# Kernel optimization log

Measured on AMD Instinct MI355X. Metric: run time of the kernel, lower is better.

## Reference

```python
import jax, jax.numpy as jnp
import numpy as np

P, M, DG, F, H, DH = 2000, 150, 2000, 256, 4, 64
N1, N2 = P + M, P + DG          # adj1 nodes (patient+med), adj2 nodes (patient+diag)
E1, E2, EGP, EGM = 137600, 256000, 64000, 4800
GNN_LAYERS = 2
SA_HID = 128


def setup_inputs() -> dict:
    key = jax.random.key(0)
    ks = jax.random.split(key, 32)
    ri = lambda k, n, hi: jax.random.randint(k, (n,), 0, hi, dtype=jnp.int32)
    rn = lambda k, shape, scale: (jax.random.normal(k, shape, dtype=jnp.float32) * scale)
    inp = {
        'adj1_rows': ri(ks[0], E1, N1), 'adj1_cols': ri(ks[1], E1, N1),
        'adj1_vals': jax.random.uniform(ks[2], (E1,), dtype=jnp.float32),
        'adj2_rows': ri(ks[3], E2, N2), 'adj2_cols': ri(ks[4], E2, N2),
        'adj2_vals': jax.random.uniform(ks[5], (E2,), dtype=jnp.float32),
        'g0_src': ri(ks[6], EGP, P), 'g0_dst': ri(ks[7], EGP, P),
        'g1_src': ri(ks[8], EGP, P), 'g1_dst': ri(ks[9], EGP, P),
        'g2_src': ri(ks[10], EGM, M), 'g2_dst': ri(ks[11], EGM, M),
        'g3_src': ri(ks[12], EGM, M), 'g3_dst': ri(ks[13], EGM, M),
        'keepRate': 1,
        # learned parameters (xavier-ish scales)
        'pEmbed': rn(ks[14], (P, F), 0.05),
        'mEmbed': rn(ks[15], (M, F), 0.05),
        'dEmbed': rn(ks[16], (DG, F), 0.05),
        'gat_W': rn(ks[17], (4, F, H * DH), (2.0 / (F + H * DH)) ** 0.5),
        'gat_al': rn(ks[18], (4, H, DH), 0.1),
        'gat_ar': rn(ks[19], (4, H, DH), 0.1),
        'gat_b': jnp.zeros((4, H * DH), dtype=jnp.float32),
        'sa_W1': rn(ks[20], (H * DH, SA_HID), (2.0 / (H * DH + SA_HID)) ** 0.5),
        'sa_b1': jnp.zeros((SA_HID,), dtype=jnp.float32),
        'sa_W2': rn(ks[21], (SA_HID, 1), 0.1),
        'out_W': rn(ks[22], (2 * F, M), (2.0 / (2 * F + M)) ** 0.5),
        'out_b': jnp.zeros((M,), dtype=jnp.float32),
    }
    return inp


def _spmm(rows, cols, vals, x, n):
    # sparse adj @ x via gather + segment_sum
    return jax.ops.segment_sum(vals[:, None] * x[cols], rows, num_segments=n)


def _seg_softmax(e, seg, n):
    m = jax.ops.segment_max(e, seg, num_segments=n)          # [n, H]
    ex = jnp.exp(e - m[seg])
    s = jax.ops.segment_sum(ex, seg, num_segments=n)
    return ex / (s[seg] + 1e-9)


def _gat(h, W, al, ar, b, src, dst, n):
    # DGL GATConv, feat/attn dropout = 0, negative_slope = 0.2, activation = elu
    feat = (h @ W).reshape(n, H, DH)                          # [n, H, DH]
    el = (feat * al[None]).sum(-1)                            # [n, H]
    er = (feat * ar[None]).sum(-1)
    e = jax.nn.leaky_relu(el[src] + er[dst], negative_slope=0.2)  # [E, H]
    alpha = _seg_softmax(e, dst, n)                           # softmax over in-edges per dst
    out = jax.ops.segment_sum(alpha[:, :, None] * feat[src], dst, num_segments=n)
    out = out + b.reshape(1, H, DH)
    return jax.nn.elu(out).reshape(n, H * DH)


def _sem_att(z, W1, b1, W2):
    # z: [N, K, F]; shared projection; beta over K meta-paths
    w = (jnp.tanh(z @ W1 + b1) @ W2).mean(0)                  # [K, 1]
    beta = jax.nn.softmax(w, axis=0)                          # [K, 1]
    return (beta[None] * z).sum(1)                            # [N, F]


def reference(adj1_rows, adj1_cols, adj1_vals, adj2_rows, adj2_cols, adj2_vals,
              g0_src, g0_dst, g1_src, g1_dst, g2_src, g2_dst, g3_src, g3_dst,
              keepRate, pEmbed, mEmbed, dEmbed, gat_W, gat_al, gat_ar, gat_b,
              sa_W1, sa_b1, sa_W2, out_W, out_b):
    embeds1 = jnp.concatenate([pEmbed, mEmbed], axis=0)       # [N1, F]
    embeds2 = jnp.concatenate([pEmbed, dEmbed], axis=0)       # [N2, F]
    lat1, lat2 = embeds1, embeds2
    acc1 = jnp.zeros_like(embeds1)
    acc2 = jnp.zeros_like(embeds2)
    for _ in range(GNN_LAYERS):
        lat1 = jax.nn.leaky_relu(_spmm(adj1_rows, adj1_cols, adj1_vals, lat1, N1), negative_slope=0.5)
        lat2 = jax.nn.leaky_relu(_spmm(adj2_rows, adj2_cols, adj2_vals, lat2, N2), negative_slope=0.5)
        acc1 = acc1 + lat1
        acc2 = acc2 + lat2
    p1, m_gcn = acc1[:P], acc1[P:]
    p2, d_gcn = acc2[:P], acc2[P:]

    e0 = _gat(p1, gat_W[0], gat_al[0], gat_ar[0], gat_b[0], g0_src, g0_dst, P)
    e1 = _gat(p2, gat_W[1], gat_al[1], gat_ar[1], gat_b[1], g1_src, g1_dst, P)
    e2 = _gat(m_gcn, gat_W[2], gat_al[2], gat_ar[2], gat_b[2], g2_src, g2_dst, M)
    e3 = _gat(m_gcn, gat_W[3], gat_al[3], gat_ar[3], gat_b[3], g3_src, g3_dst, M)

    patient = _sem_att(jnp.stack([e0, e1], axis=1), sa_W1, sa_b1, sa_W2)  # [P, F]
    med = _sem_att(jnp.stack([e2, e3], axis=1), sa_W1, sa_b1, sa_W2)      # [M, F]

    # broadcasted pairwise concat -> ReLU -> Linear -> sum over pairing axis
    pm = jnp.concatenate([
        jnp.broadcast_to(patient[:, None, :], (P, M, F)),
        jnp.broadcast_to(med[None, :, :], (P, M, F)),
    ], axis=-1).reshape(P * M, 2 * F)
    simi = (jax.nn.relu(pm) @ out_W + out_b).reshape(P, M, M)
    simi_pm = simi.sum(axis=1)                                # [P, M]
    return (simi_pm, d_gcn, med, m_gcn, patient)
```

## Files before the change

kernel.cpp:

```cpp
#include <hip/hip_runtime.h>
#include <cmath>
#include <cstdint>

constexpr int P  = 2000, M = 150, DG = 2000, F = 256, H = 4, DH = 64;
constexpr int N1 = P + M;
constexpr int N2 = P + DG;
constexpr int E1 = 137600, E2 = 256000, EGP = 64000, EGM = 4800;
constexpr int SA_HID = 128;

constexpr int HO1 = E1, HO2 = E1 + E2, HO3 = HO2 + EGP, HO4 = HO3 + EGP,
              HO5 = HO4 + EGM, HOE = HO5 + EGM;

__global__ void k_hist_all(const int* __restrict__ a1r, const int* __restrict__ a2r,
                           const int* __restrict__ d0, const int* __restrict__ d1,
                           const int* __restrict__ d2, const int* __restrict__ d3,
                           int* __restrict__ c1, int* __restrict__ c2,
                           int* __restrict__ cg0, int* __restrict__ cg1,
                           int* __restrict__ cg2, int* __restrict__ cg3) {
  int i = blockIdx.x * 256 + threadIdx.x;
  if (i >= HOE) return;
  if (i < HO1)      atomicAdd(&c1[a1r[i]], 1);
  else if (i < HO2) atomicAdd(&c2[a2r[i - HO1]], 1);
  else if (i < HO3) atomicAdd(&cg0[d0[i - HO2]], 1);
  else if (i < HO4) atomicAdd(&cg1[d1[i - HO3]], 1);
  else if (i < HO5) atomicAdd(&cg2[d2[i - HO4]], 1);
  else              atomicAdd(&cg3[d3[i - HO5]], 1);
}

struct ScanArgs { const int* cnt[6]; int* off[6]; int* cur[6]; int n[6]; };

__global__ void k_scan_all(ScanArgs a) {
  int b = blockIdx.x;
  const int* cnt = a.cnt[b]; int* off = a.off[b]; int* cur = a.cur[b]; int n = a.n[b];
  __shared__ int part[256];
  int t = threadIdx.x;
  int chunk = (n + 255) >> 8;
  int base = t * chunk;
  int s = 0;
  for (int i = 0; i < chunk; ++i) { int id = base + i; if (id < n) s += cnt[id]; }
  part[t] = s;
  __syncthreads();
  for (int d = 1; d < 256; d <<= 1) {
    int v = (t >= d) ? part[t - d] : 0;
    __syncthreads();
    part[t] += v;
    __syncthreads();
  }
  int run = (t == 0) ? 0 : part[t - 1];
  for (int i = 0; i < chunk; ++i) {
    int id = base + i;
    if (id < n) { off[id] = run; cur[id] = run; run += cnt[id]; }
  }
  if (t == 0) off[n] = part[255];
}

__global__ void k_scat_all(const int* __restrict__ a1r, const int* __restrict__ a1c,
                           const float* __restrict__ a1v,
                           const int* __restrict__ a2r, const int* __restrict__ a2c,
                           const float* __restrict__ a2v,
                           const int* __restrict__ d0, const int* __restrict__ s0,
                           const int* __restrict__ d1, const int* __restrict__ s1,
                           const int* __restrict__ d2, const int* __restrict__ s2,
                           const int* __restrict__ d3, const int* __restrict__ s3,
                           int* cur1, int* pc1, float* pv1,
                           int* cur2, int* pc2, float* pv2,
                           int* cu0, int* ps0, int* cu1, int* ps1,
                           int* cu2, int* ps2, int* cu3, int* ps3) {
  int i = blockIdx.x * 256 + threadIdx.x;
  if (i >= HOE) return;
  if (i < HO1) {
    int p = atomicAdd(&cur1[a1r[i]], 1); pc1[p] = a1c[i]; pv1[p] = a1v[i];
  } else if (i < HO2) {
    int j = i - HO1;
    int p = atomicAdd(&cur2[a2r[j]], 1); pc2[p] = a2c[j]; pv2[p] = a2v[j];
  } else if (i < HO3) {
    int j = i - HO2; int p = atomicAdd(&cu0[d0[j]], 1); ps0[p] = s0[j];
  } else if (i < HO4) {
    int j = i - HO3; int p = atomicAdd(&cu1[d1[j]], 1); ps1[p] = s1[j];
  } else if (i < HO5) {
    int j = i - HO4; int p = atomicAdd(&cu2[d2[j]], 1); ps2[p] = s2[j];
  } else {
    int j = i - HO5; int p = atomicAdd(&cu3[d3[j]], 1); ps3[p] = s3[j];
  }
}

template<int LAYER>
__global__ __launch_bounds__(256) void k_spmm(
    const int* __restrict__ off1, const int* __restrict__ pc1, const float* __restrict__ pv1,
    const int* __restrict__ off2, const int* __restrict__ pc2, const float* __restrict__ pv2,
    const float* __restrict__ pE, const float* __restrict__ mE, const float* __restrict__ dE,
    float* __restrict__ lat1, float* __restrict__ lat2,
    float* __restrict__ acc1, float* __restrict__ acc2,
    float* __restrict__ out_mgcn, float* __restrict__ out_dgcn) {
  int gw = (blockIdx.x * 256 + threadIdx.x) >> 6;
  if (gw >= N1 + N2) return;
  int lane = threadIdx.x & 63;
  bool g2 = gw >= N1;
  int row = g2 ? gw - N1 : gw;
  const int*   off = g2 ? off2 : off1;
  const int*   pc  = g2 ? pc2  : pc1;
  const float* pv  = g2 ? pv2  : pv1;
  const float* latin = g2 ? lat2 : lat1;
  const float* tailE = g2 ? dE : mE;
  int beg = off[row], end = off[row + 1];
  int fo = lane << 2;
  float4 s = {0.f, 0.f, 0.f, 0.f};
  auto fetch = [&](int c) -> float4 {
    const float* b;
    if (LAYER == 1) b = (c < P) ? (pE + (size_t)c * F) : (tailE + (size_t)(c - P) * F);
    else            b = latin + (size_t)c * F;
    return *(const float4*)(b + fo);
  };
  int i = beg;
  for (; i + 4 <= end; i += 4) {
    int c0 = pc[i], c1 = pc[i + 1], c2 = pc[i + 2], c3 = pc[i + 3];
    float v0 = pv[i], v1 = pv[i + 1], v2 = pv[i + 2], v3 = pv[i + 3];
    float4 a0 = fetch(c0), a1 = fetch(c1), a2 = fetch(c2), a3 = fetch(c3);
    s.x += v0 * a0.x + v1 * a1.x + v2 * a2.x + v3 * a3.x;
    s.y += v0 * a0.y + v1 * a1.y + v2 * a2.y + v3 * a3.y;
    s.z += v0 * a0.z + v1 * a1.z + v2 * a2.z + v3 * a3.z;
    s.w += v0 * a0.w + v1 * a1.w + v2 * a2.w + v3 * a3.w;
  }
  for (; i < end; ++i) {
    int c = pc[i]; float v = pv[i];
    float4 a = fetch(c);
    s.x += v * a.x; s.y += v * a.y; s.z += v * a.z; s.w += v * a.w;
  }
  float4 l;
  l.x = s.x > 0.f ? s.x : 0.5f * s.x;
  l.y = s.y > 0.f ? s.y : 0.5f * s.y;
  l.z = s.z > 0.f ? s.z : 0.5f * s.z;
  l.w = s.w > 0.f ? s.w : 0.5f * s.w;
  if (LAYER == 1) {
    *(float4*)((g2 ? lat2 : lat1) + (size_t)row * F + fo) = l;
  } else {
    float4 b = *(const float4*)(latin + (size_t)row * F + fo);
    float4 a = {b.x + l.x, b.y + l.y, b.z + l.z, b.w + l.w};
    *(float4*)((g2 ? acc2 : acc1) + (size_t)row * F + fo) = a;
    if (row >= P)
      *(float4*)((g2 ? out_dgcn : out_mgcn) + (size_t)(row - P) * F + fo) = a;
  }
}

constexpr int FR  = 4;
constexpr int NB0 = (P + FR - 1) / FR;
constexpr int NB2 = (M + FR - 1) / FR;
constexpr int FEAT_BLOCKS = 2 * NB0 + 2 * NB2;

__global__ __launch_bounds__(256) void k_gat_feat_all(
    const float* __restrict__ acc1, const float* __restrict__ acc2,
    const float* __restrict__ gat_W, const float* __restrict__ gat_al,
    const float* __restrict__ gat_ar,
    float* __restrict__ f0, float* __restrict__ f1,
    float* __restrict__ f2, float* __restrict__ f3,
    float* __restrict__ el, float* __restrict__ er) {
  int b = blockIdx.x;
  int g, rb, n; const float* h; float* fout;
  if (b < NB0)            { g = 0; rb = b;              n = P; h = acc1; fout = f0; }
  else if (b < 2 * NB0)   { g = 1; rb = b - NB0;        n = P; h = acc2; fout = f1; }
  else if (b < 2*NB0+NB2) { g = 2; rb = b - 2 * NB0;    n = M; h = acc1 + (size_t)P * F; fout = f2; }
  else                    { g = 3; rb = b - 2*NB0 - NB2; n = M; h = acc1 + (size_t)P * F; fout = f3; }
  int elo = (g == 0) ? 0 : (g == 1) ? P * H : (g == 2) ? 2 * P * H : (2 * P + M) * H;
  const float* W = gat_W + (size_t)g * F * F;
  __shared__ float hs[FR][F];
  int t = threadIdx.x;
  int r0 = rb * FR;
  {
    int r = t >> 6, ln = t & 63;
    int row = r0 + r;
    float4 v = {0.f, 0.f, 0.f, 0.f};
    if (row < n) v = *(const float4*)(h + (size_t)row * F + (ln << 2));
    *(float4*)&hs[r][ln << 2] = v;
  }
  __syncthreads();
  float acc[FR] = {0.f, 0.f, 0.f, 0.f};
  for (int k = 0; k < F; k += 4) {
    float w0 = W[(size_t)k * F + t],       w1 = W[(size_t)(k + 1) * F + t],
          w2 = W[(size_t)(k + 2) * F + t], w3 = W[(size_t)(k + 3) * F + t];
#pragma unroll
    for (int r = 0; r < FR; ++r) {
      float4 h4 = *(const float4*)&hs[r][k];
      acc[r] += h4.x * w0 + h4.y * w1 + h4.z * w2 + h4.w * w3;
    }
  }
  int head = t >> 6, d = t & 63;
  float av = gat_al[g * H * DH + head * DH + d];
  float rv = gat_ar[g * H * DH + head * DH + d];
#pragma unroll
  for (int r = 0; r < FR; ++r) {
    int row = r0 + r;
    if (row < n) {
      fout[(size_t)row * F + t] = acc[r];
      float cl = acc[r] * av, cr = acc[r] * rv;
      for (int o = 32; o > 0; o >>= 1) {
        cl += __shfl_down(cl, o, 64);
        cr += __shfl_down(cr, o, 64);
      }
      if (d == 0) { el[elo + row * H + head] = cl; er[elo + row * H + head] = cr; }
    }
  }
}

__global__ __launch_bounds__(256) void k_gat_agg_all(
    const int* __restrict__ og0, const int* __restrict__ ps0,
    const int* __restrict__ og1, const int* __restrict__ ps1,
    const int* __restrict__ og2, const int* __restrict__ ps2,
    const int* __restrict__ og3, const int* __restrict__ ps3,
    const float* __restrict__ el, const float* __restrict__ er,
    const float* __restrict__ f0, const float* __restrict__ f1,
    const float* __restrict__ f2, const float* __restrict__ f3,
    const float* __restrict__ gat_b,
    float* __restrict__ e0, float* __restrict__ e1,
    float* __restrict__ e2, float* __restrict__ e3) {
  int gw = (blockIdx.x * 256 + threadIdx.x) >> 6;
  if (gw >= 2 * P + 2 * M) return;
  int lane = threadIdx.x & 63;
  int g, row; const int* off; const int* ps; const float* feat; float* out; int elo;
  if (gw < P)            { g = 0; row = gw;             off = og0; ps = ps0; feat = f0; out = e0; elo = 0; }
  else if (gw < 2 * P)   { g = 1; row = gw - P;         off = og1; ps = ps1; feat = f1; out = e1; elo = P * H; }
  else if (gw < 2*P + M) { g = 2; row = gw - 2 * P;     off = og2; ps = ps2; feat = f2; out = e2; elo = 2 * P * H; }
  else                   { g = 3; row = gw - 2 * P - M; off = og3; ps = ps3; feat = f3; out = e3; elo = (2 * P + M) * H; }
  int head = lane >> 4;
  int fo = lane << 2;
  const float* elb = el + elo;
  float erv = er[elo + row * H + head];
  int beg = off[row], end = off[row + 1];
  float mx = -3.4e38f;
  int i = beg;
  for (; i + 4 <= end; i += 4) {
    int s0 = ps[i], s1 = ps[i + 1], s2 = ps[i + 2], s3 = ps[i + 3];
    float a = elb[s0 * H + head] + erv, b = elb[s1 * H + head] + erv,
          c = elb[s2 * H + head] + erv, d = elb[s3 * H + head] + erv;
    a = a > 0.f ? a : 0.2f * a; b = b > 0.f ? b : 0.2f * b;
    c = c > 0.f ? c : 0.2f * c; d = d > 0.f ? d : 0.2f * d;
    mx = fmaxf(mx, fmaxf(fmaxf(a, b), fmaxf(c, d)));
  }
  for (; i < end; ++i) {
    float a = elb[ps[i] * H + head] + erv;
    a = a > 0.f ? a : 0.2f * a;
    mx = fmaxf(mx, a);
  }
  float ssum = 0.f;
  float4 acc = {0.f, 0.f, 0.f, 0.f};
  i = beg;
  for (; i + 2 <= end; i += 2) {
    int s0 = ps[i], s1 = ps[i + 1];
    float a = elb[s0 * H + head] + erv; a = a > 0.f ? a : 0.2f * a;
    float b = elb[s1 * H + head] + erv; b = b > 0.f ? b : 0.2f * b;
    float x0 = expf(a - mx), x1 = expf(b - mx);
    float4 q0 = *(const float4*)(feat + (size_t)s0 * F + fo);
    float4 q1 = *(const float4*)(feat + (size_t)s1 * F + fo);
    ssum += x0 + x1;
    acc.x += x0 * q0.x + x1 * q1.x;
    acc.y += x0 * q0.y + x1 * q1.y;
    acc.z += x0 * q0.z + x1 * q1.z;
    acc.w += x0 * q0.w + x1 * q1.w;
  }
  for (; i < end; ++i) {
    int s0 = ps[i];
    float a = elb[s0 * H + head] + erv; a = a > 0.f ? a : 0.2f * a;
    float x0 = expf(a - mx);
    float4 q0 = *(const float4*)(feat + (size_t)s0 * F + fo);
    ssum += x0;
    acc.x += x0 * q0.x; acc.y += x0 * q0.y; acc.z += x0 * q0.z; acc.w += x0 * q0.w;
  }
  float inv = 1.f / (ssum + 1e-9f);
  const float* bb = gat_b + g * F + fo;
  float4 v = {acc.x * inv + bb[0], acc.y * inv + bb[1],
              acc.z * inv + bb[2], acc.w * inv + bb[3]};
  v.x = v.x > 0.f ? v.x : expm1f(v.x);
  v.y = v.y > 0.f ? v.y : expm1f(v.y);
  v.z = v.z > 0.f ? v.z : expm1f(v.z);
  v.w = v.w > 0.f ? v.w : expm1f(v.w);
  *(float4*)(out + (size_t)row * F + fo) = v;
}

constexpr int SR  = 8;
constexpr int SB0 = (P + SR - 1) / SR;
constexpr int SB2 = (M + SR - 1) / SR;
constexpr int SEM_BLOCKS = 2 * SB0 + 2 * SB2;

__global__ __launch_bounds__(128) void k_sem_w_all(
    const float* __restrict__ e0, const float* __restrict__ e1,
    const float* __restrict__ e2, const float* __restrict__ e3,
    const float* __restrict__ W1, const float* __restrict__ b1,
    const float* __restrict__ W2, float* __restrict__ w) {
  int b = blockIdx.x;
  int zid, rb, n; const float* z;
  if (b < SB0)            { zid = 0; rb = b;             n = P; z = e0; }
  else if (b < 2 * SB0)   { zid = 1; rb = b - SB0;       n = P; z = e1; }
  else if (b < 2*SB0+SB2) { zid = 2; rb = b - 2 * SB0;   n = M; z = e2; }
  else                    { zid = 3; rb = b - 2*SB0-SB2; n = M; z = e3; }
  __shared__ float zs[SR][F];
  int t = threadIdx.x;
  int r0 = rb * SR;
  for (int q = t; q < SR * 64; q += 128) {
    int r = q >> 6, ln = q & 63;
    int row = r0 + r;
    float4 v = {0.f, 0.f, 0.f, 0.f};
    if (row < n) v = *(const float4*)(z + (size_t)row * F + (ln << 2));
    *(float4*)&zs[r][ln << 2] = v;
  }
  __syncthreads();
  float hid[SR];
#pragma unroll
  for (int r = 0; r < SR; ++r) hid[r] = b1[t];
  for (int k = 0; k < F; k += 4) {
    float w0 = W1[(size_t)k * SA_HID + t],       w1 = W1[(size_t)(k + 1) * SA_HID + t],
          w2 = W1[(size_t)(k + 2) * SA_HID + t], w3 = W1[(size_t)(k + 3) * SA_HID + t];
#pragma unroll
    for (int r = 0; r < SR; ++r) {
      float4 z4 = *(const float4*)&zs[r][k];
      hid[r] += z4.x * w0 + z4.y * w1 + z4.z * w2 + z4.w * w3;
    }
  }
  float w2v = W2[t];
  float local = 0.f;
  for (int r = 0; r < SR; ++r) {
    int row = r0 + r;
    if (row < n) local += tanhf(hid[r]) * w2v;
  }
  for (int o = 32; o > 0; o >>= 1) local += __shfl_down(local, o, 64);
  __shared__ float pp[2];
  if ((t & 63) == 0) pp[t >> 6] = local;
  __syncthreads();
  if (t == 0) atomicAdd(&w[zid], pp[0] + pp[1]);
}

__global__ void k_sem_comb_all(const float* __restrict__ e0, const float* __restrict__ e1,
                               const float* __restrict__ e2, const float* __restrict__ e3,
                               const float* __restrict__ w,
                               float* __restrict__ out_pat, float* __restrict__ out_med) {
  constexpr int Q0 = P * F / 4;
  constexpr int QE = Q0 + M * F / 4;
  int i = blockIdx.x * 256 + threadIdx.x;
  if (i >= QE) return;
  const float4 *z0, *z1; float* out; float inv_n; const float* wp; int j;
  if (i < Q0) { z0 = (const float4*)e0; z1 = (const float4*)e1; out = out_pat; inv_n = 1.f / P; wp = w;     j = i; }
  else        { z0 = (const float4*)e2; z1 = (const float4*)e3; out = out_med; inv_n = 1.f / M; wp = w + 2; j = i - Q0; }
  float m0 = wp[0] * inv_n, m1 = wp[1] * inv_n;
  float mxv = fmaxf(m0, m1);
  float a0 = expf(m0 - mxv), a1 = expf(m1 - mxv);
  float s = 1.f / (a0 + a1);
  a0 *= s; a1 *= s;
  float4 u0 = z0[j], u1 = z1[j];
  float4 r = {a0 * u0.x + a1 * u1.x, a0 * u0.y + a1 * u1.y,
              a0 * u0.z + a1 * u1.z, a0 * u0.w + a1 * u1.w};
  ((float4*)out)[j] = r;
}

__global__ void k_cvec(const float* __restrict__ med, const float* __restrict__ outW,
                       const float* __restrict__ outb, float* __restrict__ c) {
  __shared__ float sv[F];
  int t = threadIdx.x;
  float a = 0.f;
  for (int m = 0; m < M; ++m) { float v = med[(size_t)m * F + t]; a += v > 0.f ? v : 0.f; }
  sv[t] = a;
  __syncthreads();
  if (t < M) {
    float cc = (float)M * outb[t];
    for (int f = 0; f < F; ++f) cc += sv[f] * outW[(size_t)(F + f) * M + t];
    c[t] = cc;
  }
}

constexpr int FIN_R = 8;
__global__ __launch_bounds__(256) void k_final(const float* __restrict__ pat,
                                               const float* __restrict__ outW,
                                               const float* __restrict__ c,
                                               float* __restrict__ simi) {
  __shared__ float psh[FIN_R][F];
  int t = threadIdx.x;
  int r0 = blockIdx.x * FIN_R;
  for (int q = t; q < FIN_R * 64; q += 256) {
    int r = q >> 6, ln = q & 63;
    float4 v = *(const float4*)(pat + (size_t)(r0 + r) * F + (ln << 2));
    v.x = v.x > 0.f ? v.x : 0.f; v.y = v.y > 0.f ? v.y : 0.f;
    v.z = v.z > 0.f ? v.z : 0.f; v.w = v.w > 0.f ? v.w : 0.f;
    *(float4*)&psh[r][ln << 2] = v;
  }
  __syncthreads();
  if (t < M) {
    float acc[FIN_R];
#pragma unroll
    for (int r = 0; r < FIN_R; ++r) acc[r] = 0.f;
    for (int f = 0; f < F; f += 4) {
      float w0 = outW[(size_t)f * M + t],       w1 = outW[(size_t)(f + 1) * M + t],
            w2 = outW[(size_t)(f + 2) * M + t], w3 = outW[(size_t)(f + 3) * M + t];
#pragma unroll
      for (int r = 0; r < FIN_R; ++r) {
        float4 p4 = *(const float4*)&psh[r][f];
        acc[r] += p4.x * w0 + p4.y * w1 + p4.z * w2 + p4.w * w3;
      }
    }
    float cv = c[t];
    for (int r = 0; r < FIN_R; ++r)
      simi[(size_t)(r0 + r) * M + t] = (float)M * acc[r] + cv;
  }
}

extern "C" void kernel_launch(void* const* d_in, const int* in_sizes, int n_in,
                              void* d_out, int out_size, void* d_ws, size_t ws_size,
                              hipStream_t stream) {
  const int*   adj1_rows = (const int*)d_in[0];
  const int*   adj1_cols = (const int*)d_in[1];
  const float* adj1_vals = (const float*)d_in[2];
  const int*   adj2_rows = (const int*)d_in[3];
  const int*   adj2_cols = (const int*)d_in[4];
  const float* adj2_vals = (const float*)d_in[5];
  const int*   g0_src = (const int*)d_in[6];
  const int*   g0_dst = (const int*)d_in[7];
  const int*   g1_src = (const int*)d_in[8];
  const int*   g1_dst = (const int*)d_in[9];
  const int*   g2_src = (const int*)d_in[10];
  const int*   g2_dst = (const int*)d_in[11];
  const int*   g3_src = (const int*)d_in[12];
  const int*   g3_dst = (const int*)d_in[13];
  const float* pE     = (const float*)d_in[15];
  const float* mE     = (const float*)d_in[16];
  const float* dE     = (const float*)d_in[17];
  const float* gat_W  = (const float*)d_in[18];
  const float* gat_al = (const float*)d_in[19];
  const float* gat_ar = (const float*)d_in[20];
  const float* gat_b  = (const float*)d_in[21];
  const float* sa_W1  = (const float*)d_in[22];
  const float* sa_b1  = (const float*)d_in[23];
  const float* sa_W2  = (const float*)d_in[24];
  const float* out_W  = (const float*)d_in[25];
  const float* out_b  = (const float*)d_in[26];

  int* ip = (int*)d_ws;
  int* cnt1 = ip; ip += N1;
  int* cnt2 = ip; ip += N2;
  int* cg0  = ip; ip += P;
  int* cg1  = ip; ip += P;
  int* cg2  = ip; ip += M;
  int* cg3  = ip; ip += M;
  float* wbuf = (float*)ip; ip += 4;
  size_t memset_bytes = (size_t)((char*)ip - (char*)d_ws);
  int* off1 = ip; ip += N1 + 1;  int* cur1 = ip; ip += N1;
  int* pc1  = ip; ip += E1;      float* pv1 = (float*)ip; ip += E1;
  int* off2 = ip; ip += N2 + 1;  int* cur2 = ip; ip += N2;
  int* pc2  = ip; ip += E2;      float* pv2 = (float*)ip; ip += E2;
  int* og0 = ip; ip += P + 1;  int* cu0 = ip; ip += P;  int* ps0 = ip; ip += EGP;
  int* og1 = ip; ip += P + 1;  int* cu1 = ip; ip += P;  int* ps1 = ip; ip += EGP;
  int* og2 = ip; ip += M + 1;  int* cu2 = ip; ip += M;  int* ps2 = ip; ip += EGM;
  int* og3 = ip; ip += M + 1;  int* cu3 = ip; ip += M;  int* ps3 = ip; ip += EGM;
  uintptr_t up = ((uintptr_t)ip + 15) & ~(uintptr_t)15;
  float* fp = (float*)up;
  float* lat1 = fp; fp += (size_t)N1 * F;
  float* lat2 = fp; fp += (size_t)N2 * F;
  float* acc1 = fp; fp += (size_t)N1 * F;
  float* acc2 = fp; fp += (size_t)N2 * F;
  float* f0   = fp; fp += (size_t)P * F;
  float* f1   = fp; fp += (size_t)P * F;
  float* f2   = fp; fp += (size_t)M * F;
  float* f3   = fp; fp += (size_t)M * F;
  float* el   = fp; fp += (size_t)(2 * P + 2 * M) * H;
  float* er   = fp; fp += (size_t)(2 * P + 2 * M) * H;
  float* e0b  = fp; fp += (size_t)P * F;
  float* e1b  = fp; fp += (size_t)P * F;
  float* e2b  = fp; fp += (size_t)M * F;
  float* e3b  = fp; fp += (size_t)M * F;
  float* cbuf = fp; fp += 256;

  float* out_simi = (float*)d_out;
  float* out_dgcn = out_simi + (size_t)P * M;
  float* out_med  = out_dgcn + (size_t)DG * F;
  float* out_mgcn = out_med  + (size_t)M * F;
  float* out_pat  = out_mgcn + (size_t)M * F;

  hipMemsetAsync(d_ws, 0, memset_bytes, stream);

  int eb = (HOE + 255) / 256;
  k_hist_all<<<eb, 256, 0, stream>>>(adj1_rows, adj2_rows, g0_dst, g1_dst, g2_dst, g3_dst,
                                     cnt1, cnt2, cg0, cg1, cg2, cg3);
  ScanArgs sa;
  sa.cnt[0] = cnt1; sa.off[0] = off1; sa.cur[0] = cur1; sa.n[0] = N1;
  sa.cnt[1] = cnt2; sa.off[1] = off2; sa.cur[1] = cur2; sa.n[1] = N2;
  sa.cnt[2] = cg0;  sa.off[2] = og0;  sa.cur[2] = cu0;  sa.n[2] = P;
  sa.cnt[3] = cg1;  sa.off[3] = og1;  sa.cur[3] = cu1;  sa.n[3] = P;
  sa.cnt[4] = cg2;  sa.off[4] = og2;  sa.cur[4] = cu2;  sa.n[4] = M;
  sa.cnt[5] = cg3;  sa.off[5] = og3;  sa.cur[5] = cu3;  sa.n[5] = M;
  k_scan_all<<<6, 256, 0, stream>>>(sa);
  k_scat_all<<<eb, 256, 0, stream>>>(adj1_rows, adj1_cols, adj1_vals,
                                     adj2_rows, adj2_cols, adj2_vals,
                                     g0_dst, g0_src, g1_dst, g1_src,
                                     g2_dst, g2_src, g3_dst, g3_src,
                                     cur1, pc1, pv1, cur2, pc2, pv2,
                                     cu0, ps0, cu1, ps1, cu2, ps2, cu3, ps3);

  int sb = ((N1 + N2) * 64 + 255) / 256;
  k_spmm<1><<<sb, 256, 0, stream>>>(off1, pc1, pv1, off2, pc2, pv2, pE, mE, dE,
                                    lat1, lat2, acc1, acc2, out_mgcn, out_dgcn);
  k_spmm<2><<<sb, 256, 0, stream>>>(off1, pc1, pv1, off2, pc2, pv2, pE, mE, dE,
                                    lat1, lat2, acc1, acc2, out_mgcn, out_dgcn);

  k_gat_feat_all<<<FEAT_BLOCKS, 256, 0, stream>>>(acc1, acc2, gat_W, gat_al, gat_ar,
                                                  f0, f1, f2, f3, el, er);
  int ab = ((2 * P + 2 * M) * 64 + 255) / 256;
  k_gat_agg_all<<<ab, 256, 0, stream>>>(og0, ps0, og1, ps1, og2, ps2, og3, ps3,
                                        el, er, f0, f1, f2, f3, gat_b,
                                        e0b, e1b, e2b, e3b);

  k_sem_w_all<<<SEM_BLOCKS, 128, 0, stream>>>(e0b, e1b, e2b, e3b, sa_W1, sa_b1, sa_W2, wbuf);
  int cb = ((P * F + M * F) / 4 + 255) / 256;
  k_sem_comb_all<<<cb, 256, 0, stream>>>(e0b, e1b, e2b, e3b, wbuf, out_pat, out_med);

  k_cvec<<<1, 256, 0, stream>>>(out_med, out_W, out_b, cbuf);
  k_final<<<P / FIN_R, 256, 0, stream>>>(out_pat, out_W, cbuf, out_simi);
}
```

Baseline: 364.4 us.

## Replace CSR build with fixed-capacity ELL plus overflow, fuse cvec into combine

The three-kernel CSR construction (histogram, scan, scatter) becomes a single pass that scatters edges into fixed-capacity per-row ELL slots, with a global overflow list for rows whose degree exceeds the cap. The SpMM and GAT aggregation kernels read the ELL rows and also scan the overflow list. Separately, the constant-vector kernel is folded into the semantic-combine kernel through a last-block-done atomic counter. This removes two launches and the serial scan, at the cost of larger padded buffers, strided row storage, and a linear overflow scan that every row pays whenever overflow occurs.

```diff
diff --git a/kernel.cpp b/kernel.cpp
--- a/kernel.cpp
+++ b/kernel.cpp
@@ -11,83 +11,64 @@
 constexpr int HO1 = E1, HO2 = E1 + E2, HO3 = HO2 + EGP, HO4 = HO3 + EGP,
               HO5 = HO4 + EGM, HOE = HO5 + EGM;
 
-__global__ void k_hist_all(const int* __restrict__ a1r, const int* __restrict__ a2r,
-                           const int* __restrict__ d0, const int* __restrict__ d1,
-                           const int* __restrict__ d2, const int* __restrict__ d3,
-                           int* __restrict__ c1, int* __restrict__ c2,
-                           int* __restrict__ cg0, int* __restrict__ cg1,
-                           int* __restrict__ cg2, int* __restrict__ cg3) {
-  int i = blockIdx.x * 256 + threadIdx.x;
-  if (i >= HOE) return;
-  if (i < HO1)      atomicAdd(&c1[a1r[i]], 1);
-  else if (i < HO2) atomicAdd(&c2[a2r[i - HO1]], 1);
-  else if (i < HO3) atomicAdd(&cg0[d0[i - HO2]], 1);
-  else if (i < HO4) atomicAdd(&cg1[d1[i - HO3]], 1);
-  else if (i < HO5) atomicAdd(&cg2[d2[i - HO4]], 1);
-  else              atomicAdd(&cg3[d3[i - HO5]], 1);
-}
-
-struct ScanArgs { const int* cnt[6]; int* off[6]; int* cur[6]; int n[6]; };
-
-__global__ void k_scan_all(ScanArgs a) {
-  int b = blockIdx.x;
-  const int* cnt = a.cnt[b]; int* off = a.off[b]; int* cur = a.cur[b]; int n = a.n[b];
-  __shared__ int part[256];
-  int t = threadIdx.x;
-  int chunk = (n + 255) >> 8;
-  int base = t * chunk;
-  int s = 0;
-  for (int i = 0; i < chunk; ++i) { int id = base + i; if (id < n) s += cnt[id]; }
-  part[t] = s;
-  __syncthreads();
-  for (int d = 1; d < 256; d <<= 1) {
-    int v = (t >= d) ? part[t - d] : 0;
-    __syncthreads();
-    part[t] += v;
-    __syncthreads();
-  }
-  int run = (t == 0) ? 0 : part[t - 1];
-  for (int i = 0; i < chunk; ++i) {
-    int id = base + i;
-    if (id < n) { off[id] = run; cur[id] = run; run += cnt[id]; }
-  }
-  if (t == 0) off[n] = part[255];
-}
-
-__global__ void k_scat_all(const int* __restrict__ a1r, const int* __restrict__ a1c,
-                           const float* __restrict__ a1v,
-                           const int* __restrict__ a2r, const int* __restrict__ a2c,
-                           const float* __restrict__ a2v,
-                           const int* __restrict__ d0, const int* __restrict__ s0,
-                           const int* __restrict__ d1, const int* __restrict__ s1,
-                           const int* __restrict__ d2, const int* __restrict__ s2,
-                           const int* __restrict__ d3, const int* __restrict__ s3,
-                           int* cur1, int* pc1, float* pv1,
-                           int* cur2, int* pc2, float* pv2,
-                           int* cu0, int* ps0, int* cu1, int* ps1,
-                           int* cu2, int* ps2, int* cu3, int* ps3) {
+constexpr int CAP_A = 160;
+constexpr int CAP_G = 96;
+constexpr int OVF_CAP = 4096;
+
+__global__ __launch_bounds__(256) void k_build(
+    const int* __restrict__ a1r, const int* __restrict__ a1c, const float* __restrict__ a1v,
+    const int* __restrict__ a2r, const int* __restrict__ a2c, const float* __restrict__ a2v,
+    const int* __restrict__ d0, const int* __restrict__ s0,
+    const int* __restrict__ d1, const int* __restrict__ s1,
+    const int* __restrict__ d2, const int* __restrict__ s2,
+    const int* __restrict__ d3, const int* __restrict__ s3,
+    int* cur1, uint2* ell1, int* cur2, uint2* ell2,
+    int* cu0, unsigned* eg0, int* cu1, unsigned* eg1,
+    int* cu2, unsigned* eg2, int* cu3, unsigned* eg3,
+    int* __restrict__ ovf_n, int4* __restrict__ ovf) {
   int i = blockIdx.x * 256 + threadIdx.x;
   if (i >= HOE) return;
   if (i < HO1) {
-    int p = atomicAdd(&cur1[a1r[i]], 1); pc1[p] = a1c[i]; pv1[p] = a1v[i];
+    int r = a1r[i];
+    int slot = atomicAdd(&cur1[r], 1);
+    uint2 pl = {(unsigned)a1c[i], __float_as_uint(a1v[i])};
+    if (slot < CAP_A) ell1[(size_t)r * CAP_A + slot] = pl;
+    else { int o = atomicAdd(&ovf_n[0], 1); if (o < OVF_CAP) ovf[0 * OVF_CAP + o] = make_int4(r, (int)pl.x, (int)pl.y, 0); }
   } else if (i < HO2) {
     int j = i - HO1;
-    int p = atomicAdd(&cur2[a2r[j]], 1); pc2[p] = a2c[j]; pv2[p] = a2v[j];
+    int r = a2r[j];
+    int slot = atomicAdd(&cur2[r], 1);
+    uint2 pl = {(unsigned)a2c[j], __float_as_uint(a2v[j])};
+    if (slot < CAP_A) ell2[(size_t)r * CAP_A + slot] = pl;
+    else { int o = atomicAdd(&ovf_n[1], 1); if (o < OVF_CAP) ovf[1 * OVF_CAP + o] = make_int4(r, (int)pl.x, (int)pl.y, 0); }
   } else if (i < HO3) {
-    int j = i - HO2; int p = atomicAdd(&cu0[d0[j]], 1); ps0[p] = s0[j];
+    int j = i - HO2; int r = d0[j];
+    int slot = atomicAdd(&cu0[r], 1);
+    if (slot < CAP_G) eg0[(size_t)r * CAP_G + slot] = (unsigned)s0[j];
+    else { int o = atomicAdd(&ovf_n[2], 1); if (o < OVF_CAP) ovf[2 * OVF_CAP + o] = make_int4(r, s0[j], 0, 0); }
   } else if (i < HO4) {
-    int j = i - HO3; int p = atomicAdd(&cu1[d1[j]], 1); ps1[p] = s1[j];
+    int j = i - HO3; int r = d1[j];
+    int slot = atomicAdd(&cu1[r], 1);
+    if (slot < CAP_G) eg1[(size_t)r * CAP_G + slot] = (unsigned)s1[j];
+    else { int o = atomicAdd(&ovf_n[3], 1); if (o < OVF_CAP) ovf[3 * OVF_CAP + o] = make_int4(r, s1[j], 0, 0); }
   } else if (i < HO5) {
-    int j = i - HO4; int p = atomicAdd(&cu2[d2[j]], 1); ps2[p] = s2[j];
+    int j = i - HO4; int r = d2[j];
+    int slot = atomicAdd(&cu2[r], 1);
+    if (slot < CAP_G) eg2[(size_t)r * CAP_G + slot] = (unsigned)s2[j];
+    else { int o = atomicAdd(&ovf_n[4], 1); if (o < OVF_CAP) ovf[4 * OVF_CAP + o] = make_int4(r, s2[j], 0, 0); }
   } else {
-    int j = i - HO5; int p = atomicAdd(&cu3[d3[j]], 1); ps3[p] = s3[j];
+    int j = i - HO5; int r = d3[j];
+    int slot = atomicAdd(&cu3[r], 1);
+    if (slot < CAP_G) eg3[(size_t)r * CAP_G + slot] = (unsigned)s3[j];
+    else { int o = atomicAdd(&ovf_n[5], 1); if (o < OVF_CAP) ovf[5 * OVF_CAP + o] = make_int4(r, s3[j], 0, 0); }
   }
 }
 
 template<int LAYER>
 __global__ __launch_bounds__(256) void k_spmm(
-    const int* __restrict__ off1, const int* __restrict__ pc1, const float* __restrict__ pv1,
-    const int* __restrict__ off2, const int* __restrict__ pc2, const float* __restrict__ pv2,
+    const int* __restrict__ cur1, const uint2* __restrict__ ell1,
+    const int* __restrict__ cur2, const uint2* __restrict__ ell2,
+    const int* __restrict__ ovf_n, const int4* __restrict__ ovf,
     const float* __restrict__ pE, const float* __restrict__ mE, const float* __restrict__ dE,
     float* __restrict__ lat1, float* __restrict__ lat2,
     float* __restrict__ acc1, float* __restrict__ acc2,
@@ -97,12 +78,11 @@
   int lane = threadIdx.x & 63;
   bool g2 = gw >= N1;
   int row = g2 ? gw - N1 : gw;
-  const int*   off = g2 ? off2 : off1;
-  const int*   pc  = g2 ? pc2  : pc1;
-  const float* pv  = g2 ? pv2  : pv1;
+  const uint2* pe = (g2 ? ell2 : ell1) + (size_t)row * CAP_A;
   const float* latin = g2 ? lat2 : lat1;
   const float* tailE = g2 ? dE : mE;
-  int beg = off[row], end = off[row + 1];
+  int deg = (g2 ? cur2 : cur1)[row];
+  int dn = deg < CAP_A ? deg : CAP_A;
   int fo = lane << 2;
   float4 s = {0.f, 0.f, 0.f, 0.f};
   auto fetch = [&](int c) -> float4 {
@@ -111,20 +91,38 @@
     else            b = latin + (size_t)c * F;
     return *(const float4*)(b + fo);
   };
-  int i = beg;
-  for (; i + 4 <= end; i += 4) {
-    int c0 = pc[i], c1 = pc[i + 1], c2 = pc[i + 2], c3 = pc[i + 3];
-    float v0 = pv[i], v1 = pv[i + 1], v2 = pv[i + 2], v3 = pv[i + 3];
-    float4 a0 = fetch(c0), a1 = fetch(c1), a2 = fetch(c2), a3 = fetch(c3);
+  int i = 0;
+  for (; i + 4 <= dn; i += 4) {
+    uint2 m0 = pe[i], m1 = pe[i + 1], m2 = pe[i + 2], m3 = pe[i + 3];
+    float v0 = __uint_as_float(m0.y), v1 = __uint_as_float(m1.y),
+          v2 = __uint_as_float(m2.y), v3 = __uint_as_float(m3.y);
+    float4 a0 = fetch((int)m0.x), a1 = fetch((int)m1.x),
+           a2 = fetch((int)m2.x), a3 = fetch((int)m3.x);
     s.x += v0 * a0.x + v1 * a1.x + v2 * a2.x + v3 * a3.x;
     s.y += v0 * a0.y + v1 * a1.y + v2 * a2.y + v3 * a3.y;
     s.z += v0 * a0.z + v1 * a1.z + v2 * a2.z + v3 * a3.z;
     s.w += v0 * a0.w + v1 * a1.w + v2 * a2.w + v3 * a3.w;
   }
-  for (; i < end; ++i) {
-    int c = pc[i]; float v = pv[i];
-    float4 a = fetch(c);
+  for (; i < dn; ++i) {
+    uint2 m = pe[i];
+    float v = __uint_as_float(m.y);
+    float4 a = fetch((int)m.x);
     s.x += v * a.x; s.y += v * a.y; s.z += v * a.z; s.w += v * a.w;
+  }
+  {
+    int gi = g2 ? 1 : 0;
+    int on = ovf_n[gi];
+    if (on > 0) {
+      const int4* ol = ovf + gi * OVF_CAP;
+      for (int k = 0; k < on; ++k) {
+        int4 e = ol[k];
+        if (e.x == row) {
+          float v = __int_as_float(e.z);
+          float4 a = fetch(e.y);
+          s.x += v * a.x; s.y += v * a.y; s.z += v * a.z; s.w += v * a.w;
+        }
+      }
+    }
   }
   float4 l;
   l.x = s.x > 0.f ? s.x : 0.5f * s.x;
@@ -202,10 +200,11 @@
 }
 
 __global__ __launch_bounds__(256) void k_gat_agg_all(
-    const int* __restrict__ og0, const int* __restrict__ ps0,
-    const int* __restrict__ og1, const int* __restrict__ ps1,
-    const int* __restrict__ og2, const int* __restrict__ ps2,
-    const int* __restrict__ og3, const int* __restrict__ ps3,
+    const int* __restrict__ cu0, const unsigned* __restrict__ eg0,
+    const int* __restrict__ cu1, const unsigned* __restrict__ eg1,
+    const int* __restrict__ cu2, const unsigned* __restrict__ eg2,
+    const int* __restrict__ cu3, const unsigned* __restrict__ eg3,
+    const int* __restrict__ ovf_n, const int4* __restrict__ ovf,
     const float* __restrict__ el, const float* __restrict__ er,
     const float* __restrict__ f0, const float* __restrict__ f1,
     const float* __restrict__ f2, const float* __restrict__ f3,
@@ -215,36 +214,50 @@
   int gw = (blockIdx.x * 256 + threadIdx.x) >> 6;
   if (gw >= 2 * P + 2 * M) return;
   int lane = threadIdx.x & 63;
-  int g, row; const int* off; const int* ps; const float* feat; float* out; int elo;
-  if (gw < P)            { g = 0; row = gw;             off = og0; ps = ps0; feat = f0; out = e0; elo = 0; }
-  else if (gw < 2 * P)   { g = 1; row = gw - P;         off = og1; ps = ps1; feat = f1; out = e1; elo = P * H; }
-  else if (gw < 2*P + M) { g = 2; row = gw - 2 * P;     off = og2; ps = ps2; feat = f2; out = e2; elo = 2 * P * H; }
-  else                   { g = 3; row = gw - 2 * P - M; off = og3; ps = ps3; feat = f3; out = e3; elo = (2 * P + M) * H; }
+  int g, row; const int* cu; const unsigned* eg; const float* feat; float* out; int elo;
+  if (gw < P)            { g = 0; row = gw;             cu = cu0; eg = eg0; feat = f0; out = e0; elo = 0; }
+  else if (gw < 2 * P)   { g = 1; row = gw - P;         cu = cu1; eg = eg1; feat = f1; out = e1; elo = P * H; }
+  else if (gw < 2*P + M) { g = 2; row = gw - 2 * P;     cu = cu2; eg = eg2; feat = f2; out = e2; elo = 2 * P * H; }
+  else                   { g = 3; row = gw - 2 * P - M; cu = cu3; eg = eg3; feat = f3; out = e3; elo = (2 * P + M) * H; }
   int head = lane >> 4;
   int fo = lane << 2;
   const float* elb = el + elo;
   float erv = er[elo + row * H + head];
-  int beg = off[row], end = off[row + 1];
+  int deg = cu[row];
+  int dn = deg < CAP_G ? deg : CAP_G;
+  const unsigned* ps = eg + (size_t)row * CAP_G;
+  int on = ovf_n[2 + g];
+  const int4* ol = ovf + (2 + g) * OVF_CAP;
   float mx = -3.4e38f;
-  int i = beg;
-  for (; i + 4 <= end; i += 4) {
-    int s0 = ps[i], s1 = ps[i + 1], s2 = ps[i + 2], s3 = ps[i + 3];
+  int i = 0;
+  for (; i + 4 <= dn; i += 4) {
+    int s0 = (int)ps[i], s1 = (int)ps[i + 1], s2 = (int)ps[i + 2], s3 = (int)ps[i + 3];
     float a = elb[s0 * H + head] + erv, b = elb[s1 * H + head] + erv,
           c = elb[s2 * H + head] + erv, d = elb[s3 * H + head] + erv;
     a = a > 0.f ? a : 0.2f * a; b = b > 0.f ? b : 0.2f * b;
     c = c > 0.f ? c : 0.2f * c; d = d > 0.f ? d : 0.2f * d;
     mx = fmaxf(mx, fmaxf(fmaxf(a, b), fmaxf(c, d)));
   }
-  for (; i < end; ++i) {
-    float a = elb[ps[i] * H + head] + erv;
+  for (; i < dn; ++i) {
+    float a = elb[(int)ps[i] * H + head] + erv;
     a = a > 0.f ? a : 0.2f * a;
     mx = fmaxf(mx, a);
   }
+  if (on > 0) {
+    for (int k = 0; k < on; ++k) {
+      int4 e = ol[k];
+      if (e.x == row) {
+        float a = elb[e.y * H + head] + erv;
+        a = a > 0.f ? a : 0.2f * a;
+        mx = fmaxf(mx, a);
+      }
+    }
+  }
   float ssum = 0.f;
   float4 acc = {0.f, 0.f, 0.f, 0.f};
-  i = beg;
-  for (; i + 2 <= end; i += 2) {
-    int s0 = ps[i], s1 = ps[i + 1];
+  i = 0;
+  for (; i + 2 <= dn; i += 2) {
+    int s0 = (int)ps[i], s1 = (int)ps[i + 1];
     float a = elb[s0 * H + head] + erv; a = a > 0.f ? a : 0.2f * a;
     float b = elb[s1 * H + head] + erv; b = b > 0.f ? b : 0.2f * b;
     float x0 = expf(a - mx), x1 = expf(b - mx);
@@ -256,13 +269,25 @@
     acc.z += x0 * q0.z + x1 * q1.z;
     acc.w += x0 * q0.w + x1 * q1.w;
   }
-  for (; i < end; ++i) {
-    int s0 = ps[i];
+  for (; i < dn; ++i) {
+    int s0 = (int)ps[i];
     float a = elb[s0 * H + head] + erv; a = a > 0.f ? a : 0.2f * a;
     float x0 = expf(a - mx);
     float4 q0 = *(const float4*)(feat + (size_t)s0 * F + fo);
     ssum += x0;
     acc.x += x0 * q0.x; acc.y += x0 * q0.y; acc.z += x0 * q0.z; acc.w += x0 * q0.w;
+  }
+  if (on > 0) {
+    for (int k = 0; k < on; ++k) {
+      int4 e = ol[k];
+      if (e.x == row) {
+        float a = elb[e.y * H + head] + erv; a = a > 0.f ? a : 0.2f * a;
+        float x0 = expf(a - mx);
+        float4 q0 = *(const float4*)(feat + (size_t)e.y * F + fo);
+        ssum += x0;
+        acc.x += x0 * q0.x; acc.y += x0 * q0.y; acc.z += x0 * q0.z; acc.w += x0 * q0.w;
+      }
+    }
   }
   float inv = 1.f / (ssum + 1e-9f);
   const float* bb = gat_b + g * F + fo;
@@ -327,40 +352,49 @@
   if (t == 0) atomicAdd(&w[zid], pp[0] + pp[1]);
 }
 
-__global__ void k_sem_comb_all(const float* __restrict__ e0, const float* __restrict__ e1,
-                               const float* __restrict__ e2, const float* __restrict__ e3,
-                               const float* __restrict__ w,
-                               float* __restrict__ out_pat, float* __restrict__ out_med) {
-  constexpr int Q0 = P * F / 4;
-  constexpr int QE = Q0 + M * F / 4;
+constexpr int Q0 = P * F / 4;
+constexpr int QE = Q0 + M * F / 4;
+constexpr int COMB_BLOCKS = (QE + 255) / 256;
+
+__global__ __launch_bounds__(256) void k_sem_comb_all(
+    const float* __restrict__ e0, const float* __restrict__ e1,
+    const float* __restrict__ e2, const float* __restrict__ e3,
+    const float* __restrict__ w,
+    float* __restrict__ out_pat, float* __restrict__ out_med,
+    const float* __restrict__ outW, const float* __restrict__ outb,
+    float* __restrict__ cbuf, int* __restrict__ done) {
   int i = blockIdx.x * 256 + threadIdx.x;
-  if (i >= QE) return;
-  const float4 *z0, *z1; float* out; float inv_n; const float* wp; int j;
-  if (i < Q0) { z0 = (const float4*)e0; z1 = (const float4*)e1; out = out_pat; inv_n = 1.f / P; wp = w;     j = i; }
-  else        { z0 = (const float4*)e2; z1 = (const float4*)e3; out = out_med; inv_n = 1.f / M; wp = w + 2; j = i - Q0; }
-  float m0 = wp[0] * inv_n, m1 = wp[1] * inv_n;
-  float mxv = fmaxf(m0, m1);
-  float a0 = expf(m0 - mxv), a1 = expf(m1 - mxv);
-  float s = 1.f / (a0 + a1);
-  a0 *= s; a1 *= s;
-  float4 u0 = z0[j], u1 = z1[j];
-  float4 r = {a0 * u0.x + a1 * u1.x, a0 * u0.y + a1 * u1.y,
-              a0 * u0.z + a1 * u1.z, a0 * u0.w + a1 * u1.w};
-  ((float4*)out)[j] = r;
-}
-
-__global__ void k_cvec(const float* __restrict__ med, const float* __restrict__ outW,
-                       const float* __restrict__ outb, float* __restrict__ c) {
+  if (i < QE) {
+    const float4 *z0, *z1; float* out; float inv_n; const float* wp; int j;
+    if (i < Q0) { z0 = (const float4*)e0; z1 = (const float4*)e1; out = out_pat; inv_n = 1.f / P; wp = w;     j = i; }
+    else        { z0 = (const float4*)e2; z1 = (const float4*)e3; out = out_med; inv_n = 1.f / M; wp = w + 2; j = i - Q0; }
+    float m0 = wp[0] * inv_n, m1 = wp[1] * inv_n;
+    float mxv = fmaxf(m0, m1);
+    float a0 = expf(m0 - mxv), a1 = expf(m1 - mxv);
+    float s = 1.f / (a0 + a1);
+    a0 *= s; a1 *= s;
+    float4 u0 = z0[j], u1 = z1[j];
+    float4 r = {a0 * u0.x + a1 * u1.x, a0 * u0.y + a1 * u1.y,
+                a0 * u0.z + a1 * u1.z, a0 * u0.w + a1 * u1.w};
+    ((float4*)out)[j] = r;
+  }
+  __threadfence();
+  __syncthreads();
+  __shared__ int last;
+  if (threadIdx.x == 0) last = (atomicAdd(done, 1) == gridDim.x - 1) ? 1 : 0;
+  __syncthreads();
+  if (!last) return;
+  __threadfence();
   __shared__ float sv[F];
   int t = threadIdx.x;
   float a = 0.f;
-  for (int m = 0; m < M; ++m) { float v = med[(size_t)m * F + t]; a += v > 0.f ? v : 0.f; }
+  for (int m = 0; m < M; ++m) { float v = out_med[(size_t)m * F + t]; a += v > 0.f ? v : 0.f; }
   sv[t] = a;
   __syncthreads();
   if (t < M) {
     float cc = (float)M * outb[t];
     for (int f = 0; f < F; ++f) cc += sv[f] * outW[(size_t)(F + f) * M + t];
-    c[t] = cc;
+    cbuf[t] = cc;
   }
 }
 
@@ -430,24 +464,26 @@
   const float* out_b  = (const float*)d_in[26];
 
   int* ip = (int*)d_ws;
-  int* cnt1 = ip; ip += N1;
-  int* cnt2 = ip; ip += N2;
-  int* cg0  = ip; ip += P;
-  int* cg1  = ip; ip += P;
-  int* cg2  = ip; ip += M;
-  int* cg3  = ip; ip += M;
+  int* cur1 = ip; ip += N1;
+  int* cur2 = ip; ip += N2;
+  int* cu0  = ip; ip += P;
+  int* cu1  = ip; ip += P;
+  int* cu2  = ip; ip += M;
+  int* cu3  = ip; ip += M;
+  int* ovf_n = ip; ip += 6;
+  int* done  = ip; ip += 1;
   float* wbuf = (float*)ip; ip += 4;
   size_t memset_bytes = (size_t)((char*)ip - (char*)d_ws);
-  int* off1 = ip; ip += N1 + 1;  int* cur1 = ip; ip += N1;
-  int* pc1  = ip; ip += E1;      float* pv1 = (float*)ip; ip += E1;
-  int* off2 = ip; ip += N2 + 1;  int* cur2 = ip; ip += N2;
-  int* pc2  = ip; ip += E2;      float* pv2 = (float*)ip; ip += E2;
-  int* og0 = ip; ip += P + 1;  int* cu0 = ip; ip += P;  int* ps0 = ip; ip += EGP;
-  int* og1 = ip; ip += P + 1;  int* cu1 = ip; ip += P;  int* ps1 = ip; ip += EGP;
-  int* og2 = ip; ip += M + 1;  int* cu2 = ip; ip += M;  int* ps2 = ip; ip += EGM;
-  int* og3 = ip; ip += M + 1;  int* cu3 = ip; ip += M;  int* ps3 = ip; ip += EGM;
+
   uintptr_t up = ((uintptr_t)ip + 15) & ~(uintptr_t)15;
-  float* fp = (float*)up;
+  int4* ovf = (int4*)up;
+  uint2* ell1 = (uint2*)(ovf + 6 * OVF_CAP);
+  uint2* ell2 = ell1 + (size_t)N1 * CAP_A;
+  unsigned* eg0 = (unsigned*)(ell2 + (size_t)N2 * CAP_A);
+  unsigned* eg1 = eg0 + (size_t)P * CAP_G;
+  unsigned* eg2 = eg1 + (size_t)P * CAP_G;
+  unsigned* eg3 = eg2 + (size_t)M * CAP_G;
+  float* fp = (float*)(eg3 + (size_t)M * CAP_G);
   float* lat1 = fp; fp += (size_t)N1 * F;
   float* lat2 = fp; fp += (size_t)N2 * F;
   float* acc1 = fp; fp += (size_t)N1 * F;
@@ -473,40 +509,31 @@
   hipMemsetAsync(d_ws, 0, memset_bytes, stream);
 
   int eb = (HOE + 255) / 256;
-  k_hist_all<<<eb, 256, 0, stream>>>(adj1_rows, adj2_rows, g0_dst, g1_dst, g2_dst, g3_dst,
-                                     cnt1, cnt2, cg0, cg1, cg2, cg3);
-  ScanArgs sa;
-  sa.cnt[0] = cnt1; sa.off[0] = off1; sa.cur[0] = cur1; sa.n[0] = N1;
-  sa.cnt[1] = cnt2; sa.off[1] = off2; sa.cur[1] = cur2; sa.n[1] = N2;
-  sa.cnt[2] = cg0;  sa.off[2] = og0;  sa.cur[2] = cu0;  sa.n[2] = P;
-  sa.cnt[3] = cg1;  sa.off[3] = og1;  sa.cur[3] = cu1;  sa.n[3] = P;
-  sa.cnt[4] = cg2;  sa.off[4] = og2;  sa.cur[4] = cu2;  sa.n[4] = M;
-  sa.cnt[5] = cg3;  sa.off[5] = og3;  sa.cur[5] = cu3;  sa.n[5] = M;
-  k_scan_all<<<6, 256, 0, stream>>>(sa);
-  k_scat_all<<<eb, 256, 0, stream>>>(adj1_rows, adj1_cols, adj1_vals,
-                                     adj2_rows, adj2_cols, adj2_vals,
-                                     g0_dst, g0_src, g1_dst, g1_src,
-                                     g2_dst, g2_src, g3_dst, g3_src,
-                                     cur1, pc1, pv1, cur2, pc2, pv2,
-                                     cu0, ps0, cu1, ps1, cu2, ps2, cu3, ps3);
+  k_build<<<eb, 256, 0, stream>>>(adj1_rows, adj1_cols, adj1_vals,
+                                  adj2_rows, adj2_cols, adj2_vals,
+                                  g0_dst, g0_src, g1_dst, g1_src,
+                                  g2_dst, g2_src, g3_dst, g3_src,
+                                  cur1, ell1, cur2, ell2,
+                                  cu0, eg0, cu1, eg1, cu2, eg2, cu3, eg3,
+                                  ovf_n, ovf);
 
   int sb = ((N1 + N2) * 64 + 255) / 256;
-  k_spmm<1><<<sb, 256, 0, stream>>>(off1, pc1, pv1, off2, pc2, pv2, pE, mE, dE,
+  k_spmm<1><<<sb, 256, 0, stream>>>(cur1, ell1, cur2, ell2, ovf_n, ovf, pE, mE, dE,
                                     lat1, lat2, acc1, acc2, out_mgcn, out_dgcn);
-  k_spmm<2><<<sb, 256, 0, stream>>>(off1, pc1, pv1, off2, pc2, pv2, pE, mE, dE,
+  k_spmm<2><<<sb, 256, 0, stream>>>(cur1, ell1, cur2, ell2, ovf_n, ovf, pE, mE, dE,
                                     lat1, lat2, acc1, acc2, out_mgcn, out_dgcn);
 
   k_gat_feat_all<<<FEAT_BLOCKS, 256, 0, stream>>>(acc1, acc2, gat_W, gat_al, gat_ar,
                                                   f0, f1, f2, f3, el, er);
   int ab = ((2 * P + 2 * M) * 64 + 255) / 256;
-  k_gat_agg_all<<<ab, 256, 0, stream>>>(og0, ps0, og1, ps1, og2, ps2, og3, ps3,
-                                        el, er, f0, f1, f2, f3, gat_b,
+  k_gat_agg_all<<<ab, 256, 0, stream>>>(cu0, eg0, cu1, eg1, cu2, eg2, cu3, eg3,
+                                        ovf_n, ovf, el, er, f0, f1, f2, f3, gat_b,
                                         e0b, e1b, e2b, e3b);
 
   k_sem_w_all<<<SEM_BLOCKS, 128, 0, stream>>>(e0b, e1b, e2b, e3b, sa_W1, sa_b1, sa_W2, wbuf);
-  int cb = ((P * F + M * F) / 4 + 255) / 256;
-  k_sem_comb_all<<<cb, 256, 0, stream>>>(e0b, e1b, e2b, e3b, wbuf, out_pat, out_med);
-
-  k_cvec<<<1, 256, 0, stream>>>(out_med, out_W, out_b, cbuf);
+  k_sem_comb_all<<<COMB_BLOCKS, 256, 0, stream>>>(e0b, e1b, e2b, e3b, wbuf,
+                                                  out_pat, out_med, out_W, out_b,
+                                                  cbuf, done);
+
   k_final<<<P / FIN_R, 256, 0, stream>>>(out_pat, out_W, cbuf, out_simi);
 }
```

Measured after the change: 362.3 us. No clear change (-0.6%).
